# Kernel tuning notes

Measured on AMD Instinct MI355X. Metric: run time of the kernel, lower is better.

Reference implementation:

```python
import jax, jax.numpy as jnp
import numpy as np

OHNM_RATIO = 30
DEFAULT_NEG_PERC = 0.1
EPS = 1e-10


def setup_inputs() -> dict:
    key = jax.random.key(0)
    k1, k2 = jax.random.split(key)
    shape = (1, 1, 256, 256, 256)  # (B, C, D, H, W) 3D segmentation volume
    preds = jax.random.normal(k1, shape, dtype=jnp.float32)  # raw logits
    targs = (jax.random.uniform(k2, shape, dtype=jnp.float32) < 1e-3).astype(jnp.int32)
    return {"preds": preds, "targs": targs}


def reference(preds, targs):
    t = targs.astype(preds.dtype)
    # elementwise BCE-with-logits: log(1 + e^x) - x * t  (numerically stable via logaddexp)
    losses = jnp.logaddexp(0.0, preds) - preds * t
    pf, tf, lf = preds.ravel(), t.ravel(), losses.ravel()

    # --- data-dependent hard-negative count (mirrors torch .item() host sync) ---
    n_pos = int(np.asarray(tf.sum()))
    n_neg = tf.size - n_pos
    n_hns = int(DEFAULT_NEG_PERC * n_neg) if n_pos == 0 else min(n_pos * OHNM_RATIO, n_neg)

    # mask out positives, take top-k hardest negatives over the flattened loss map
    masked = jnp.where(tf == 1.0, 0.0, lf)
    _, hns_idxs = jax.lax.top_k(masked, n_hns)
    # positive indices (data-dependent size, like torch.nonzero)
    pos_idxs = jnp.asarray(np.nonzero(np.asarray(tf) == 1.0)[0], dtype=hns_idxs.dtype)
    idxs = jnp.concatenate([hns_idxs, pos_idxs])  # [n_hns + n_pos]

    # gather selected samples, view as (B, C, -1) with B = C = 1
    ps = jax.nn.sigmoid(pf[idxs])[None, None, :]  # dice normalizes preds
    ts = tf[idxs][None, None, :]

    # Dice loss over dims 2+ (here the single flattened sample dim)
    inter = jnp.sum(ps * ts, axis=-1)              # [B, C]
    denom = jnp.sum(ps, axis=-1) + jnp.sum(ts, axis=-1)
    dice = jnp.mean(1.0 - (2.0 * inter + EPS) / (denom + EPS))

    return dice + jnp.mean(lf[idxs])
```

## Files before the change

kernel.cpp:

```cpp
#include <hip/hip_runtime.h>

#define EPSF 1e-10f

constexpr unsigned KEY15 = 0xBFC00000u;
constexpr int BUCK0 = 0xBFC;
constexpr int NB2   = 4096 - BUCK0;
constexpr int NBKT  = 4096;
constexpr int NREP  = 8;
constexpr int LHSZ  = NB2 + 64;
constexpr int NGRP  = 64;

typedef float pf4 __attribute__((ext_vector_type(4)));
typedef int   pi4 __attribute__((ext_vector_type(4)));

constexpr int DONE_OFF = 0;
constexpr int GCNT_OFF = 16;
constexpr int STAT_OFF = GCNT_OFF + NGRP * 16;
constexpr int REP_OFF  = STAT_OFF + NGRP * 16;
constexpr int LOW_OFF  = REP_OFF + NREP * NB2;
constexpr int ZERO_TOT = LOW_OFF + NBKT;

__device__ __forceinline__ float sigmoidf_(float x) {
    return 1.0f / (1.0f + expf(-x));
}
__device__ __forceinline__ float softplusf_(float x) {
    return fmaxf(x, 0.0f) + log1pf(expf(-fabsf(x)));
}
__device__ __forceinline__ unsigned f2key(float x) {
    unsigned b = __float_as_uint(x);
    return b ^ ((unsigned)((int)b >> 31) | 0x80000000u);
}
__device__ __forceinline__ float key2f(unsigned k) {
    unsigned b = (k & 0x80000000u) ? (k & 0x7FFFFFFFu) : ~k;
    return __uint_as_float(b);
}
__device__ __forceinline__ unsigned cload(const unsigned* p) {
    return __hip_atomic_load(p, __ATOMIC_RELAXED, __HIP_MEMORY_SCOPE_AGENT);
}

__global__ void zeroAll(unsigned* ws) {
    int stride = gridDim.x * 256;
    for (int i = blockIdx.x * 256 + threadIdx.x; i < ZERO_TOT; i += stride)
        ws[i] = 0u;
}

__global__ __launch_bounds__(256) void fused(const float* __restrict__ preds,
                                             const int* __restrict__ targs, int N,
                                             unsigned* __restrict__ ws,
                                             float* __restrict__ out) {
    __shared__ int lh[LHSZ];
    __shared__ float rp[4], rs[4], rl[4], rq[4];
    __shared__ unsigned histH[NB2];
    __shared__ unsigned sa[256], sb[256];
    __shared__ int sb1;
    __shared__ unsigned sr1;
    __shared__ double rds[4], rdl[4];
    __shared__ int s_last;
    __shared__ unsigned s_np, s_k, s_flag;
    __shared__ float s_psig, s_plos;

    unsigned* rep = ws + REP_OFF;
    unsigned* low = ws + LOW_OFF;

    for (int i = threadIdx.x; i < LHSZ; i += 256) lh[i] = 0;
    __syncthreads();

    float pc = 0.f, psig = 0.f, plos = 0.f;
    const int tid = threadIdx.x;
    const int lane = tid & 63;
    const int w = tid >> 6;
    const int dummy = NB2 + lane;

    int nfull = N >> 13;
    for (int grp = blockIdx.x; grp < nfull; grp += gridDim.x) {
        size_t ebase = ((size_t)grp << 13) + ((size_t)w << 11) + ((size_t)lane << 2);
        const float* pp  = preds + ebase;
        const float* pp2 = pp + 1024;
        const int*   tp  = targs + ebase;
        const int*   tp2 = tp + 1024;
        pf4 P[8]; pi4 T[8];
        asm volatile(
            "global_load_dwordx4 %0, %16, off\n\t"
            "global_load_dwordx4 %1, %16, off offset:1024\n\t"
            "global_load_dwordx4 %2, %16, off offset:2048\n\t"
            "global_load_dwordx4 %3, %16, off offset:3072\n\t"
            "global_load_dwordx4 %4, %17, off\n\t"
            "global_load_dwordx4 %5, %17, off offset:1024\n\t"
            "global_load_dwordx4 %6, %17, off offset:2048\n\t"
            "global_load_dwordx4 %7, %17, off offset:3072\n\t"
            "global_load_dwordx4 %8, %18, off\n\t"
            "global_load_dwordx4 %9, %18, off offset:1024\n\t"
            "global_load_dwordx4 %10, %18, off offset:2048\n\t"
            "global_load_dwordx4 %11, %18, off offset:3072\n\t"
            "global_load_dwordx4 %12, %19, off\n\t"
            "global_load_dwordx4 %13, %19, off offset:1024\n\t"
            "global_load_dwordx4 %14, %19, off offset:2048\n\t"
            "global_load_dwordx4 %15, %19, off offset:3072\n\t"
            "s_waitcnt vmcnt(0)"
            : "=&v"(P[0]), "=&v"(P[1]), "=&v"(P[2]), "=&v"(P[3]),
              "=&v"(P[4]), "=&v"(P[5]), "=&v"(P[6]), "=&v"(P[7]),
              "=&v"(T[0]), "=&v"(T[1]), "=&v"(T[2]), "=&v"(T[3]),
              "=&v"(T[4]), "=&v"(T[5]), "=&v"(T[6]), "=&v"(T[7])
            : "v"(pp), "v"(pp2), "v"(tp), "v"(tp2)
            : "memory");
#pragma unroll
        for (int g = 0; g < 8; g++) {
            pf4 pv = P[g]; pi4 tv = T[g];
#pragma unroll
            for (int j = 0; j < 4; j++) {
                float x = pv[j];
                unsigned key = f2key(x);
                int bkt = (int)(key >> 20) - BUCK0;
                bool q = (key >= KEY15) & (tv[j] == 0);
                int addr = q ? bkt : dummy;
                atomicAdd(&lh[addr], 1);
            }
            if (tv[0] | tv[1] | tv[2] | tv[3]) {
#pragma unroll
                for (int j = 0; j < 4; j++)
                    if (tv[j]) {
                        float x = pv[j];
                        pc += 1.f; psig += sigmoidf_(x); plos += softplusf_(x) - x;
                    }
            }
        }
    }
    if (blockIdx.x == gridDim.x - 1) {
        for (int i = (nfull << 13) + tid; i < N; i += 256) {
            float x = preds[i];
            if (targs[i]) { pc += 1.f; psig += sigmoidf_(x); plos += softplusf_(x) - x; }
            else {
                unsigned key = f2key(x);
                if (key >= KEY15) atomicAdd(&lh[(key >> 20) - BUCK0], 1);
            }
        }
    }
    __syncthreads();
    float qc = 0.f;
    unsigned* my = rep + (unsigned)(blockIdx.x & (NREP - 1)) * NB2;
    for (int i = tid; i < NB2; i += 256) {
        int c = lh[i];
        if (c) { atomicAdd(&my[i], (unsigned)c); qc += (float)c; }
    }
#pragma unroll
    for (int o = 32; o > 0; o >>= 1) {
        pc   += __shfl_down(pc, o);
        psig += __shfl_down(psig, o);
        plos += __shfl_down(plos, o);
        qc   += __shfl_down(qc, o);
    }
    if ((tid & 63) == 0) { rp[w] = pc; rs[w] = psig; rl[w] = plos; rq[w] = qc; }
    __syncthreads();
    if (tid == 0) {
        unsigned npb = (unsigned)(rp[0] + rp[1] + rp[2] + rp[3] + 0.5f);
        unsigned qcb = (unsigned)(rq[0] + rq[1] + rq[2] + rq[3] + 0.5f);
        float    psb = rs[0] + rs[1] + rs[2] + rs[3];
        float    plb = rl[0] + rl[1] + rl[2] + rl[3];
        unsigned ng  = (gridDim.x < (unsigned)NGRP) ? gridDim.x : (unsigned)NGRP;
        unsigned g   = blockIdx.x % ng;
        unsigned* line = ws + STAT_OFF + g * 16;
        atomicAdd(&line[0], npb);
        atomicAdd(&line[1], qcb);
        atomicAdd((float*)&line[2], psb);
        atomicAdd((float*)&line[3], plb);
        asm volatile("s_waitcnt vmcnt(0)" ::: "memory");
        unsigned expect = (gridDim.x - 1u - g) / ng + 1u;
        unsigned t = atomicAdd(&ws[GCNT_OFF + g * 16], 1u);
        int lastflag = 0;
        if (t == expect - 1u) {
            unsigned d = atomicAdd(&ws[DONE_OFF], 1u);
            lastflag = (d == ng - 1u);
        }
        s_last = lastflag;
    }
    __syncthreads();
    if (!s_last) return;

    if (tid < 64) {
        const unsigned* line = ws + STAT_OFF + tid * 16;
        unsigned np_ = cload(&line[0]);
        unsigned qc_ = cload(&line[1]);
        float    ps_ = __uint_as_float(cload(&line[2]));
        float    pl_ = __uint_as_float(cload(&line[3]));
#pragma unroll
        for (int o = 32; o > 0; o >>= 1) {
            np_ += __shfl_down(np_, o);
            qc_ += __shfl_down(qc_, o);
            ps_ += __shfl_down(ps_, o);
            pl_ += __shfl_down(pl_, o);
        }
        if (tid == 0) {
            unsigned np = np_;
            unsigned nn = (unsigned)N - np;
            unsigned k = (np == 0u) ? (unsigned)(0.1 * (double)nn)
                                    : ((30u * np < nn) ? 30u * np : nn);
            s_np = np; s_psig = ps_; s_plos = pl_; s_k = k;
            s_flag = (k > qc_) ? 1u : 0u;
        }
    }
    __syncthreads();

    for (int i = tid; i < NB2; i += 256) {
        unsigned s = 0;
#pragma unroll
        for (int r = 0; r < NREP; r++) s += cload(&rep[r * NB2 + i]);
        histH[i] = s;
    }

    if (s_flag) {
        for (int i = tid; i < N; i += 256) {
            if (!targs[i]) {
                unsigned key = f2key(preds[i]);
                if (key < KEY15) atomicAdd(&low[key >> 20], 1u);
            }
        }
    }
    __syncthreads();

    {
        int t = tid;
        int base = t * 16;
        unsigned flag = s_flag;
        unsigned c[16]; unsigned tot = 0;
#pragma unroll
        for (int j = 0; j < 16; j++) {
            int b = base + j;
            unsigned s = (b >= BUCK0) ? histH[b - BUCK0] : (flag ? cload(&low[b]) : 0u);
            c[j] = s; tot += s;
        }
        sa[t] = tot;
        if (t == 0) { sb1 = NBKT; sr1 = 0u; }
        __syncthreads();
        unsigned k = s_k;
        unsigned* src = sa; unsigned* dst = sb;
        for (int off = 1; off < 256; off <<= 1) {
            unsigned v = src[t] + ((t + off < 256) ? src[t + off] : 0u);
            dst[t] = v;
            __syncthreads();
            unsigned* tmp = src; src = dst; dst = tmp;
        }
        if (k > 0u) {
            unsigned above = src[t] - tot;
            if (above < k && above + tot >= k) {
                unsigned cum = above;
                for (int j = 15; j >= 0; j--) {
                    unsigned cc = c[j];
                    if (cum + cc >= k) { sb1 = base + j; sr1 = k - cum; break; }
                    cum += cc;
                }
            }
        }
        __syncthreads();
        int b1 = sb1; unsigned r1 = sr1;
        double ssig = 0.0, ssp = 0.0;
#pragma unroll
        for (int j = 0; j < 16; j++) {
            int b = base + j; unsigned cc = c[j];
            if (cc == 0u) continue;
            bool full = (b > b1);
            bool part = (b == b1) && (r1 > 0u);
            if (!(full || part)) continue;
            float lo = key2f((unsigned)b << 20);
            float hi = (b == NBKT - 1) ? key2f(0xFF7FFFFFu)
                                       : key2f(((unsigned)(b + 1)) << 20);
            if (full) {
                float mid = 0.5f * (lo + hi);
                ssig += (double)cc * (double)sigmoidf_(mid);
                ssp  += (double)cc * (double)softplusf_(mid);
            } else {
                unsigned take = (r1 < cc) ? r1 : cc;
                double q = (double)take / (double)cc;
                float rpv = (float)((double)hi - 0.5 * q * ((double)hi - (double)lo));
                ssig += (double)take * (double)sigmoidf_(rpv);
                ssp  += (double)take * (double)softplusf_(rpv);
            }
        }
#pragma unroll
        for (int o = 32; o > 0; o >>= 1) {
            ssig += __shfl_down(ssig, o);
            ssp  += __shfl_down(ssp, o);
        }
        if ((t & 63) == 0) { rds[w] = ssig; rdl[w] = ssp; }
        __syncthreads();
        if (t == 0) {
            double sns = rds[0] + rds[1] + rds[2] + rds[3];
            double snl = rdl[0] + rdl[1] + rdl[2] + rdl[3];
            unsigned np = s_np;
            float psig2 = s_psig, plos2 = s_plos;
            double denom = (double)psig2 + sns + (double)np;
            double dice = 1.0 - (2.0 * (double)psig2 + (double)EPSF) / (denom + (double)EPSF);
            unsigned totsel = np + k;
            double mean = totsel ? (((double)plos2 + snl) / (double)totsel) : 0.0;
            out[0] = (float)(dice + mean);
        }
    }
}

extern "C" void kernel_launch(void* const* d_in, const int* in_sizes, int n_in,
                              void* d_out, int out_size, void* d_ws, size_t ws_size,
                              hipStream_t stream) {
    const float* preds = (const float*)d_in[0];
    const int*   targs = (const int*)d_in[1];
    float* out = (float*)d_out;
    int N = in_sizes[0];
    unsigned* ws = (unsigned*)d_ws;

    int nfull = N >> 13;
    int grid = nfull + ((N & 8191) ? 1 : 0);
    if (grid < 1) grid = 1;
    if (grid > 4096) grid = 4096;

    zeroAll<<<64, 256, 0, stream>>>(ws);
    fused<<<grid, 256, 0, stream>>>(preds, targs, N, ws, out);
}
```

Baseline: 160.4 us.

## Split fused kernel into scan and single-block finalize kernels

Replaces the last-block-done atomic counter protocol with a separate single-block finalize kernel launched after the scan kernel. The replicated histogram layout is transposed so each bucket's replicas are contiguous, letting the finalize read them with two vector loads instead of eight strided atomic loads. This removes the per-block completion atomics and wait, and the scattered finalize reads. In exchange it adds an extra kernel launch and its fixed latency, and puts the scan blocks' histogram atomics for one bucket on the same cache line.

After: 168.8 us. +5.2%, slower.

```diff
diff --git a/kernel.cpp b/kernel.cpp
--- a/kernel.cpp
+++ b/kernel.cpp
@@ -13,11 +13,9 @@
 typedef float pf4 __attribute__((ext_vector_type(4)));
 typedef int   pi4 __attribute__((ext_vector_type(4)));
 
-constexpr int DONE_OFF = 0;
-constexpr int GCNT_OFF = 16;
-constexpr int STAT_OFF = GCNT_OFF + NGRP * 16;
+constexpr int STAT_OFF = 0;
 constexpr int REP_OFF  = STAT_OFF + NGRP * 16;
-constexpr int LOW_OFF  = REP_OFF + NREP * NB2;
+constexpr int LOW_OFF  = REP_OFF + NB2 * NREP;
 constexpr int ZERO_TOT = LOW_OFF + NBKT;
 
 __device__ __forceinline__ float sigmoidf_(float x) {
@@ -33,9 +31,6 @@
 __device__ __forceinline__ float key2f(unsigned k) {
     unsigned b = (k & 0x80000000u) ? (k & 0x7FFFFFFFu) : ~k;
     return __uint_as_float(b);
-}
-__device__ __forceinline__ unsigned cload(const unsigned* p) {
-    return __hip_atomic_load(p, __ATOMIC_RELAXED, __HIP_MEMORY_SCOPE_AGENT);
 }
 
 __global__ void zeroAll(unsigned* ws) {
@@ -44,23 +39,13 @@
         ws[i] = 0u;
 }
 
-__global__ __launch_bounds__(256) void fused(const float* __restrict__ preds,
+__global__ __launch_bounds__(256) void scanK(const float* __restrict__ preds,
                                              const int* __restrict__ targs, int N,
-                                             unsigned* __restrict__ ws,
-                                             float* __restrict__ out) {
+                                             unsigned* __restrict__ ws) {
     __shared__ int lh[LHSZ];
     __shared__ float rp[4], rs[4], rl[4], rq[4];
-    __shared__ unsigned histH[NB2];
-    __shared__ unsigned sa[256], sb[256];
-    __shared__ int sb1;
-    __shared__ unsigned sr1;
-    __shared__ double rds[4], rdl[4];
-    __shared__ int s_last;
-    __shared__ unsigned s_np, s_k, s_flag;
-    __shared__ float s_psig, s_plos;
 
     unsigned* rep = ws + REP_OFF;
-    unsigned* low = ws + LOW_OFF;
 
     for (int i = threadIdx.x; i < LHSZ; i += 256) lh[i] = 0;
     __syncthreads();
@@ -137,10 +122,10 @@
     }
     __syncthreads();
     float qc = 0.f;
-    unsigned* my = rep + (unsigned)(blockIdx.x & (NREP - 1)) * NB2;
+    const int rsel = blockIdx.x & (NREP - 1);
     for (int i = tid; i < NB2; i += 256) {
         int c = lh[i];
-        if (c) { atomicAdd(&my[i], (unsigned)c); qc += (float)c; }
+        if (c) { atomicAdd(&rep[i * NREP + rsel], (unsigned)c); qc += (float)c; }
     }
 #pragma unroll
     for (int o = 32; o > 0; o >>= 1) {
@@ -163,25 +148,30 @@
         atomicAdd(&line[1], qcb);
         atomicAdd((float*)&line[2], psb);
         atomicAdd((float*)&line[3], plb);
-        asm volatile("s_waitcnt vmcnt(0)" ::: "memory");
-        unsigned expect = (gridDim.x - 1u - g) / ng + 1u;
-        unsigned t = atomicAdd(&ws[GCNT_OFF + g * 16], 1u);
-        int lastflag = 0;
-        if (t == expect - 1u) {
-            unsigned d = atomicAdd(&ws[DONE_OFF], 1u);
-            lastflag = (d == ng - 1u);
-        }
-        s_last = lastflag;
-    }
-    __syncthreads();
-    if (!s_last) return;
+    }
+}
+
+__global__ __launch_bounds__(256) void finalizeK(const float* __restrict__ preds,
+                                                 const int* __restrict__ targs, int N,
+                                                 const unsigned* __restrict__ ws,
+                                                 float* __restrict__ out) {
+    __shared__ unsigned histH[NB2];
+    __shared__ unsigned sa[256], sb[256];
+    __shared__ int sb1;
+    __shared__ unsigned sr1;
+    __shared__ double rds[4], rdl[4];
+    __shared__ unsigned s_np, s_k, s_flag;
+    __shared__ float s_psig, s_plos;
+
+    const unsigned* rep = ws + REP_OFF;
+    const unsigned* low = ws + LOW_OFF;
+    const int tid = threadIdx.x;
+    const int w = tid >> 6;
 
     if (tid < 64) {
-        const unsigned* line = ws + STAT_OFF + tid * 16;
-        unsigned np_ = cload(&line[0]);
-        unsigned qc_ = cload(&line[1]);
-        float    ps_ = __uint_as_float(cload(&line[2]));
-        float    pl_ = __uint_as_float(cload(&line[3]));
+        uint4 v = *(const uint4*)(ws + STAT_OFF + tid * 16);
+        unsigned np_ = v.x, qc_ = v.y;
+        float ps_ = __uint_as_float(v.z), pl_ = __uint_as_float(v.w);
 #pragma unroll
         for (int o = 32; o > 0; o >>= 1) {
             np_ += __shfl_down(np_, o);
@@ -198,24 +188,23 @@
             s_flag = (k > qc_) ? 1u : 0u;
         }
     }
+    for (int i = tid; i < NB2; i += 256) {
+        const uint4* p = (const uint4*)(rep + i * NREP);
+        uint4 a = p[0], b = p[1];
+        histH[i] = ((a.x + a.y) + (a.z + a.w)) + ((b.x + b.y) + (b.z + b.w));
+    }
     __syncthreads();
 
-    for (int i = tid; i < NB2; i += 256) {
-        unsigned s = 0;
-#pragma unroll
-        for (int r = 0; r < NREP; r++) s += cload(&rep[r * NB2 + i]);
-        histH[i] = s;
-    }
-
     if (s_flag) {
+        unsigned* loww = (unsigned*)low;
         for (int i = tid; i < N; i += 256) {
             if (!targs[i]) {
                 unsigned key = f2key(preds[i]);
-                if (key < KEY15) atomicAdd(&low[key >> 20], 1u);
-            }
-        }
-    }
-    __syncthreads();
+                if (key < KEY15) atomicAdd(&loww[key >> 20], 1u);
+            }
+        }
+        __syncthreads();
+    }
 
     {
         int t = tid;
@@ -225,7 +214,7 @@
 #pragma unroll
         for (int j = 0; j < 16; j++) {
             int b = base + j;
-            unsigned s = (b >= BUCK0) ? histH[b - BUCK0] : (flag ? cload(&low[b]) : 0u);
+            unsigned s = (b >= BUCK0) ? histH[b - BUCK0] : (flag ? low[b] : 0u);
             c[j] = s; tot += s;
         }
         sa[t] = tot;
@@ -311,5 +300,6 @@
     if (grid > 4096) grid = 4096;
 
     zeroAll<<<64, 256, 0, stream>>>(ws);
-    fused<<<grid, 256, 0, stream>>>(preds, targs, N, ws, out);
-}
+    scanK<<<grid, 256, 0, stream>>>(preds, targs, N, ws);
+    finalizeK<<<1, 256, 0, stream>>>(preds, targs, N, ws, out);
+}
```
